# Kernel tuning notes

Measured on AMD Instinct MI355X. Metric: run time of the kernel, lower is better.

## Reference

```python
import jax, jax.numpy as jnp
import numpy as np

U, I, D = 100000, 50000, 64
N = U + I
E = 3_000_000
B = 8192
NEG_SLOPE = 0.2
REG_LAMBDA = 1e-4


def setup_inputs() -> dict:
    key = jax.random.key(0)
    ks = jax.random.split(key, 16)
    s = 0.05  # xavier-ish scale for params
    inp = {
        "user": jax.random.randint(ks[0], (B,), 0, U, dtype=jnp.int32),
        "positive": jax.random.randint(ks[1], (B,), 0, I, dtype=jnp.int32),
        "negative": jax.random.randint(ks[2], (B,), 0, I, dtype=jnp.int32),
        "rows": jax.random.randint(ks[3], (E,), 0, N, dtype=jnp.int32),
        "cols": jax.random.randint(ks[4], (E,), 0, N, dtype=jnp.int32),
        # normalized adjacency values are small positive numbers ~ 1/sqrt(du*di)
        "vals": jax.random.uniform(ks[5], (E,), dtype=jnp.float32) * 0.05,
        "user_emb": jax.random.normal(ks[6], (U, D), dtype=jnp.float32) * s,
        "item_emb": jax.random.normal(ks[7], (I, D), dtype=jnp.float32) * s,
        "W_gcn0": jax.random.normal(ks[8], (D, D), dtype=jnp.float32) * s,
        "b_gcn0": jax.random.normal(ks[9], (1, D), dtype=jnp.float32) * s,
        "W_mlp0": jax.random.normal(ks[10], (D, D), dtype=jnp.float32) * s,
        "b_mlp0": jax.random.normal(ks[11], (1, D), dtype=jnp.float32) * s,
        "W_gcn1": jax.random.normal(ks[12], (D, D), dtype=jnp.float32) * s,
        "b_gcn1": jax.random.normal(ks[13], (1, D), dtype=jnp.float32) * s,
        "W_mlp1": jax.random.normal(ks[14], (D, D), dtype=jnp.float32) * s,
        "b_mlp1": jax.random.normal(ks[15], (1, D), dtype=jnp.float32) * s,
    }
    return inp


def reference(user, positive, negative, rows, cols, vals,
              user_emb, item_emb,
              W_gcn0, b_gcn0, W_mlp0, b_mlp0,
              W_gcn1, b_gcn1, W_mlp1, b_mlp1):
    def spmm(x):  # sparse (N,N) @ dense (N,D) via COO gather + segment-sum
        return jax.ops.segment_sum(vals[:, None] * x[cols], rows, num_segments=N)

    ego = jnp.concatenate([user_emb, item_emb], axis=0)  # [N, D]
    all_embs = [ego]
    for W_g, b_g, W_m, b_m in ((W_gcn0, b_gcn0, W_mlp0, b_mlp0),
                               (W_gcn1, b_gcn1, W_mlp1, b_mlp1)):
        side = spmm(ego)
        gcn = jax.nn.leaky_relu(side @ W_g + b_g, negative_slope=NEG_SLOPE)
        ego = gcn @ W_m + b_m  # mess_dropout prob = 0 -> identity
        norm = jnp.linalg.norm(ego, axis=1, keepdims=True)
        all_embs.append(ego / jnp.maximum(norm, 1e-12))  # F.normalize p=2
    final = jnp.concatenate(all_embs, axis=1)  # [N, 3*D]
    users_e, items_e = final[:U], final[U:]

    u = users_e[user]
    p = items_e[positive]
    n = items_e[negative]
    pos_s = jnp.sum(u * p, axis=-1)
    neg_s = jnp.sum(u * n, axis=-1)
    bpr_loss = jnp.mean(jax.nn.softplus(neg_s - pos_s))  # -mean(logsigmoid(pos-neg))

    eu = user_emb[user]
    ep = item_emb[positive]
    en = item_emb[negative]
    reg = 0.5 * (jnp.sum(eu ** 2) + jnp.sum(ep ** 2) + jnp.sum(en ** 2)) / B
    reg_loss = REG_LAMBDA * reg
    return jnp.stack([bpr_loss, reg_loss])
```

## Files before the change

### kernel.cpp

```cpp
#include <hip/hip_runtime.h>
#include <math.h>

#define U_CNT 100000
#define I_CNT 50000
#define D_DIM 64
#define N_CNT 150000
#define B_CNT 8192
#define NEG_SLOPE 0.2f
#define REG_LAMBDA 1e-4f

#define RPB 128
#define NBK ((N_CNT + RPB - 1) / RPB)
#define CAP 4096

__device__ __forceinline__ float bf2f(unsigned short u) {
    return __uint_as_float((unsigned int)u << 16);
}
__device__ __forceinline__ unsigned short f2bf(float f) {
    unsigned int x = __float_as_uint(f);
    x += 0x7FFFu + ((x >> 16) & 1u);
    return (unsigned short)(x >> 16);
}

__global__ __launch_bounds__(256) void k_cvt(const float* __restrict__ uemb,
                                             const float* __restrict__ iemb,
                                             unsigned short* __restrict__ dst) {
    long long i = (long long)blockIdx.x * 256 + threadIdx.x;
    long long base = i * 8;
    const long long TOT = (long long)N_CNT * 64;
    if (base >= TOT) return;
    const long long USZ = (long long)U_CNT * 64;
    const float* s = (base < USZ) ? uemb + base : iemb + (base - USZ);
    float4 a = *(const float4*)s;
    float4 b = *(const float4*)(s + 4);
    union { unsigned short us[8]; uint4 v; } o;
    o.us[0] = f2bf(a.x); o.us[1] = f2bf(a.y); o.us[2] = f2bf(a.z); o.us[3] = f2bf(a.w);
    o.us[4] = f2bf(b.x); o.us[5] = f2bf(b.y); o.us[6] = f2bf(b.z); o.us[7] = f2bf(b.w);
    *(uint4*)(dst + base) = o.v;
}


__global__ __launch_bounds__(256) void k_bhist(const int* __restrict__ rows,
                                               int* __restrict__ bcnt, int E) {
    __shared__ int h[NBK];
    for (int i = threadIdx.x; i < NBK; i += 256) h[i] = 0;
    __syncthreads();
    int per = (E + gridDim.x - 1) / gridDim.x;
    int s = blockIdx.x * per, e = min(E, s + per);
    for (int i = s + threadIdx.x; i < e; i += 256) atomicAdd(&h[rows[i] >> 7], 1);
    __syncthreads();
    for (int i = threadIdx.x; i < NBK; i += 256) {
        int v = h[i];
        if (v) atomicAdd(&bcnt[i], v);
    }
}

__global__ void k_bscan(const int* __restrict__ bcnt, int* __restrict__ bb, int n) {
    __shared__ int lds[256];
    __shared__ int base;
    int tid = threadIdx.x;
    if (tid == 0) { base = 0; bb[0] = 0; }
    __syncthreads();
    for (int start = 0; start < n; start += 256) {
        int i = start + tid;
        int x = (i < n) ? bcnt[i] : 0;
        lds[tid] = x;
        __syncthreads();
        for (int off = 1; off < 256; off <<= 1) {
            int t = (tid >= off) ? lds[tid - off] : 0;
            __syncthreads();
            lds[tid] += t;
            __syncthreads();
        }
        if (i < n) bb[i + 1] = base + lds[tid];
        __syncthreads();
        if (tid == 0) base += lds[255];
        __syncthreads();
    }
}

__global__ __launch_bounds__(256) void k_bscatterA(const int* __restrict__ rows,
                                                   const int* __restrict__ cols,
                                                   const float* __restrict__ vals,
                                                   const int* __restrict__ bb,
                                                   int* __restrict__ bfill,
                                                   int2* __restrict__ edges, int E) {
    __shared__ int h[NBK];
    __shared__ int f[NBK];
    for (int i = threadIdx.x; i < NBK; i += 256) { h[i] = 0; f[i] = 0; }
    __syncthreads();
    int per = (E + gridDim.x - 1) / gridDim.x;
    int s = blockIdx.x * per, e = min(E, s + per);
    for (int i = s + threadIdx.x; i < e; i += 256) atomicAdd(&h[rows[i] >> 7], 1);
    __syncthreads();
    for (int i = threadIdx.x; i < NBK; i += 256) {
        int c = h[i];
        h[i] = c ? atomicAdd(&bfill[i], c) : 0;
    }
    __syncthreads();
    for (int i = s + threadIdx.x; i < e; i += 256) {
        int r = rows[i];
        int b = r >> 7, rl = r & 127;
        int pos = atomicAdd(&f[b], 1);
        int slot = bb[b] + h[b] + pos;
        edges[slot] = make_int2((rl << 18) | cols[i], __float_as_int(vals[i]));
    }
}

__global__ __launch_bounds__(256) void k_bfinal(int2* __restrict__ edges,
                                                const int* __restrict__ bb,
                                                int* __restrict__ rs, int E) {
    __shared__ int2 led[CAP];
    __shared__ int lcnt[RPB], lscan[RPB], lfill[RPB];
    int b = blockIdx.x;
    int s = bb[b], e = bb[b + 1];
    int nb = e - s;
    int tid = threadIdx.x;
    if (tid < RPB) { lcnt[tid] = 0; lfill[tid] = 0; }
    __syncthreads();
    for (int i = tid; i < nb; i += 256) {
        int2 ed = edges[s + i];
        if (i < CAP) led[i] = ed;
        atomicAdd(&lcnt[ed.x >> 18], 1);
    }
    __syncthreads();
    if (tid == 0) {
        int run = 0;
        for (int j = 0; j < RPB; ++j) { lscan[j] = run; run += lcnt[j]; }
    }
    __syncthreads();
    if (tid < RPB) {
        int row = b * RPB + tid;
        if (row < N_CNT) rs[row] = s + lscan[tid];
    }
    if (b == gridDim.x - 1 && tid == 0) rs[N_CNT] = E;
    int lim = min(nb, CAP);
    for (int i = tid; i < lim; i += 256) {
        int2 ed = led[i];
        int rl = ed.x >> 18;
        int pos = atomicAdd(&lfill[rl], 1);
        edges[s + lscan[rl] + pos] = make_int2(ed.x & 0x3FFFF, ed.y);
    }
    for (int base = CAP; base < nb; base += 256) {
        int i = base + tid;
        int2 ed;
        bool ok = (i < nb);
        if (ok) ed = edges[s + i];
        __syncthreads();
        if (ok) {
            int rl = ed.x >> 18;
            int pos = atomicAdd(&lfill[rl], 1);
            edges[s + lscan[rl] + pos] = make_int2(ed.x & 0x3FFFF, ed.y);
        }
        __syncthreads();
    }
}

__global__ void k_spmm(const int* __restrict__ rs, const int2* __restrict__ edges,
                       const unsigned short* __restrict__ src,
                       unsigned short* __restrict__ out_bf) {
    int gid = blockIdx.x * blockDim.x + threadIdx.x;
    int w = gid >> 6;
    int lane = gid & 63;
    if (w >= N_CNT) return;
    int s = rs[w], e = rs[w + 1];
    float acc = 0.f;
    int i = s;
    for (; i + 4 <= e; i += 4) {
        int2 e0 = edges[i], e1 = edges[i + 1], e2 = edges[i + 2], e3 = edges[i + 3];
        float a0 = bf2f(src[e0.x * 64 + lane]);
        float a1 = bf2f(src[e1.x * 64 + lane]);
        float a2 = bf2f(src[e2.x * 64 + lane]);
        float a3 = bf2f(src[e3.x * 64 + lane]);
        acc = fmaf(__int_as_float(e0.y), a0, acc);
        acc = fmaf(__int_as_float(e1.y), a1, acc);
        acc = fmaf(__int_as_float(e2.y), a2, acc);
        acc = fmaf(__int_as_float(e3.y), a3, acc);
    }
    for (; i < e; ++i) {
        int2 ed = edges[i];
        acc = fmaf(__int_as_float(ed.y), bf2f(src[ed.x * 64 + lane]), acc);
    }
    out_bf[(size_t)w * 64 + lane] = f2bf(acc);
}

template <int WRITE_BF>
__global__ __launch_bounds__(256, 1) void k_dense(const unsigned short* __restrict__ x_in,
                                                  const float* __restrict__ Wg,
                                                  const float* __restrict__ bg,
                                                  const float* __restrict__ Wm,
                                                  const float* __restrict__ bm,
                                                  float* __restrict__ out,
                                                  unsigned short* __restrict__ out_bf,
                                                  float* __restrict__ rnorm) {
    __shared__ __align__(16) float sWgT[4096];
    __shared__ __align__(16) float sWm[4096];
    __shared__ float sbg[64], sbm[64];
    int tid = threadIdx.x;
    for (int i = tid; i < 4096; i += 256) {
        int k = i >> 6, j = i & 63;
        sWgT[j * 64 + k] = Wg[i];
        sWm[i] = Wm[i];
    }
    if (tid < 64) {
        sbg[tid] = bg[tid];
        sbm[tid] = bm[tid];
    }
    __syncthreads();
    int r = blockIdx.x * 256 + tid;
    if (r >= N_CNT) return;

    float xr[64];
    const uint4* xp = (const uint4*)(x_in + (size_t)r * 64);
#pragma unroll
    for (int t = 0; t < 8; ++t) {
        uint4 q = xp[t];
        unsigned int u;
        u = q.x; xr[t * 8 + 0] = __uint_as_float(u << 16); xr[t * 8 + 1] = __uint_as_float(u & 0xFFFF0000u);
        u = q.y; xr[t * 8 + 2] = __uint_as_float(u << 16); xr[t * 8 + 3] = __uint_as_float(u & 0xFFFF0000u);
        u = q.z; xr[t * 8 + 4] = __uint_as_float(u << 16); xr[t * 8 + 5] = __uint_as_float(u & 0xFFFF0000u);
        u = q.w; xr[t * 8 + 6] = __uint_as_float(u << 16); xr[t * 8 + 7] = __uint_as_float(u & 0xFFFF0000u);
    }

    float z[64];
#pragma unroll
    for (int j = 0; j < 64; ++j) z[j] = sbm[j];

    for (int j = 0; j < 64; ++j) {
        float acc = sbg[j];
#pragma unroll
        for (int k = 0; k < 16; ++k) {
            float4 w = *(const float4*)&sWgT[j * 64 + k * 4];
            acc = fmaf(xr[k * 4 + 0], w.x, acc);
            acc = fmaf(xr[k * 4 + 1], w.y, acc);
            acc = fmaf(xr[k * 4 + 2], w.z, acc);
            acc = fmaf(xr[k * 4 + 3], w.w, acc);
        }
        float y = (acc >= 0.f) ? acc : NEG_SLOPE * acc;
#pragma unroll
        for (int k = 0; k < 16; ++k) {
            float4 w = *(const float4*)&sWm[j * 64 + k * 4];
            z[k * 4 + 0] = fmaf(y, w.x, z[k * 4 + 0]);
            z[k * 4 + 1] = fmaf(y, w.y, z[k * 4 + 1]);
            z[k * 4 + 2] = fmaf(y, w.z, z[k * 4 + 2]);
            z[k * 4 + 3] = fmaf(y, w.w, z[k * 4 + 3]);
        }
    }
    float nrm2 = 0.f;
#pragma unroll
    for (int j = 0; j < 64; ++j) nrm2 = fmaf(z[j], z[j], nrm2);
    float nrm = sqrtf(nrm2);
    float rn = 1.f / fmaxf(nrm, 1e-12f);
    rnorm[r] = rn;
    float4* op = (float4*)(out + (size_t)r * 64);
#pragma unroll
    for (int i = 0; i < 16; ++i) {
        float4 t;
        t.x = z[i * 4 + 0];
        t.y = z[i * 4 + 1];
        t.z = z[i * 4 + 2];
        t.w = z[i * 4 + 3];
        op[i] = t;
    }
    if (WRITE_BF) {
        uint4* bp = (uint4*)(out_bf + (size_t)r * 64);
#pragma unroll
        for (int t = 0; t < 8; ++t) {
            union { unsigned short us[8]; uint4 v; } o;
#pragma unroll
            for (int q = 0; q < 8; ++q) o.us[q] = f2bf(z[t * 8 + q]);
            bp[t] = o.v;
        }
    }
}

#define SCORE_BLOCKS 128
__global__ __launch_bounds__(256) void k_score(const int* __restrict__ user,
                                               const int* __restrict__ posi,
                                               const int* __restrict__ negi,
                                               const float* __restrict__ uemb,
                                               const float* __restrict__ iemb,
                                               const float* __restrict__ ego1,
                                               const float* __restrict__ rn1,
                                               const float* __restrict__ ego2,
                                               const float* __restrict__ rn2,
                                               float* __restrict__ out) {
    __shared__ float ssp[4], srg[4];
    int tid = threadIdx.x;
    int lane = tid & 63;
    int wv = tid >> 6;
    int gw = blockIdx.x * 4 + wv;
    const int NW = SCORE_BLOCKS * 4;

    float sp_acc = 0.f, rg_acc = 0.f;
    for (int w = gw; w < B_CNT; w += NW) {
        int iu = user[w], ip = posi[w], ineg = negi[w];
        size_t ru = (size_t)iu;
        size_t rp = (size_t)U_CNT + ip;
        size_t rn_ = (size_t)U_CNT + ineg;

        float u0 = uemb[(size_t)iu * 64 + lane];
        float p0 = iemb[(size_t)ip * 64 + lane];
        float n0 = iemb[(size_t)ineg * 64 + lane];
        float pos = u0 * p0;
        float neg = u0 * n0;
        float reg = u0 * u0 + p0 * p0 + n0 * n0;

        float a1 = rn1[ru], b1 = rn1[rp], c1 = rn1[rn_];
        float u1 = ego1[ru * 64 + lane] * a1;
        float p1 = ego1[rp * 64 + lane] * b1;
        float n1 = ego1[rn_ * 64 + lane] * c1;
        pos = fmaf(u1, p1, pos);
        neg = fmaf(u1, n1, neg);

        float a2 = rn2[ru], b2 = rn2[rp], c2 = rn2[rn_];
        float u2 = ego2[ru * 64 + lane] * a2;
        float p2 = ego2[rp * 64 + lane] * b2;
        float n2 = ego2[rn_ * 64 + lane] * c2;
        pos = fmaf(u2, p2, pos);
        neg = fmaf(u2, n2, neg);

#pragma unroll
        for (int off = 32; off; off >>= 1) {
            pos += __shfl_xor(pos, off);
            neg += __shfl_xor(neg, off);
            reg += __shfl_xor(reg, off);
        }
        float t = neg - pos;
        float sp = fmaxf(t, 0.f) + log1pf(expf(-fabsf(t)));
        sp_acc += sp;
        rg_acc += reg;
    }
    if (lane == 0) {
        ssp[wv] = sp_acc;
        srg[wv] = rg_acc;
    }
    __syncthreads();
    if (tid == 0) {
        float s = ssp[0] + ssp[1] + ssp[2] + ssp[3];
        float r = srg[0] + srg[1] + srg[2] + srg[3];
        atomicAdd(&out[0], s * (1.0f / B_CNT));
        atomicAdd(&out[1], r * (0.5f * REG_LAMBDA / B_CNT));
    }
}


static inline size_t alignup(size_t x) { return (x + 255) & ~(size_t)255; }

extern "C" void kernel_launch(void* const* d_in, const int* in_sizes, int n_in,
                              void* d_out, int out_size, void* d_ws, size_t ws_size,
                              hipStream_t stream) {
    const int* user = (const int*)d_in[0];
    const int* posi = (const int*)d_in[1];
    const int* negi = (const int*)d_in[2];
    const int* rows = (const int*)d_in[3];
    const int* cols = (const int*)d_in[4];
    const float* vals = (const float*)d_in[5];
    const float* uemb = (const float*)d_in[6];
    const float* iemb = (const float*)d_in[7];
    const float* Wg0 = (const float*)d_in[8];
    const float* bg0 = (const float*)d_in[9];
    const float* Wm0 = (const float*)d_in[10];
    const float* bm0 = (const float*)d_in[11];
    const float* Wg1 = (const float*)d_in[12];
    const float* bg1 = (const float*)d_in[13];
    const float* Wm1 = (const float*)d_in[14];
    const float* bm1 = (const float*)d_in[15];
    const int E = in_sizes[3];
    float* out = (float*)d_out;

    char* p = (char*)d_ws;
    auto take = [&](size_t bytes) -> char* {
        char* q = p;
        p += alignup(bytes);
        return q;
    };
    int* rs = (int*)take((size_t)(N_CNT + 1) * 4);
    int* bcnt = (int*)take((size_t)NBK * 4 * 2);
    int* bfill = bcnt + NBK;
    int* bb = (int*)take((size_t)(NBK + 1) * 4);
    int2* edges = (int2*)take((size_t)E * 8);
    unsigned short* ego0_bf = (unsigned short*)take((size_t)N_CNT * 64 * 2);
    unsigned short* side_bf = (unsigned short*)take((size_t)N_CNT * 64 * 2);
    unsigned short* ego1_bf = (unsigned short*)take((size_t)N_CNT * 64 * 2);
    float* ego1 = (float*)take((size_t)N_CNT * 64 * 4);
    float* ego2 = (float*)take((size_t)N_CNT * 64 * 4);
    float* rn1 = (float*)take((size_t)N_CNT * 4);
    float* rn2 = (float*)take((size_t)N_CNT * 4);

    hipMemsetAsync(out, 0, 2 * sizeof(float), stream);
    hipMemsetAsync(bcnt, 0, (size_t)NBK * 4 * 2, stream);

    const long long TOT = (long long)N_CNT * 64;
    int cb = (int)((TOT / 8 + 255) / 256);
    k_cvt<<<cb, 256, 0, stream>>>(uemb, iemb, ego0_bf);

    k_bhist<<<256, 256, 0, stream>>>(rows, bcnt, E);
    k_bscan<<<1, 256, 0, stream>>>(bcnt, bb, NBK);
    k_bscatterA<<<256, 256, 0, stream>>>(rows, cols, vals, bb, bfill, edges, E);
    k_bfinal<<<NBK, 256, 0, stream>>>(edges, bb, rs, E);

    int sb = (N_CNT * 64 + 255) / 256;
    int db = (N_CNT + 255) / 256;

    k_spmm<<<sb, 256, 0, stream>>>(rs, edges, ego0_bf, side_bf);
    k_dense<1><<<db, 256, 0, stream>>>(side_bf, Wg0, bg0, Wm0, bm0, ego1, ego1_bf, rn1);
    k_spmm<<<sb, 256, 0, stream>>>(rs, edges, ego1_bf, side_bf);
    k_dense<0><<<db, 256, 0, stream>>>(side_bf, Wg1, bg1, Wm1, bm1, ego2, (unsigned short*)nullptr, rn2);

    k_score<<<SCORE_BLOCKS, 256, 0, stream>>>(user, posi, negi, uemb, iemb,
                                              ego1, rn1, ego2, rn2, out);
}
```

Before: 637.9 us.

## Split SpMM wavefront into four edge groups with vectorized bf16 gathers

```diff
diff --git a/kernel.cpp b/kernel.cpp
--- a/kernel.cpp
+++ b/kernel.cpp
@@ -156,36 +156,50 @@
     }
 }
 
-__global__ void k_spmm(const int* __restrict__ rs, const int2* __restrict__ edges,
-                       const unsigned short* __restrict__ src,
-                       unsigned short* __restrict__ out_bf) {
+__global__ __launch_bounds__(256) void k_spmm(const int* __restrict__ rs,
+                                              const int2* __restrict__ edges,
+                                              const unsigned short* __restrict__ src,
+                                              unsigned short* __restrict__ out_bf) {
     int gid = blockIdx.x * blockDim.x + threadIdx.x;
     int w = gid >> 6;
-    int lane = gid & 63;
     if (w >= N_CNT) return;
+    int lane = threadIdx.x & 63;
+    int sub = lane >> 4;
+    int sl = lane & 15;
     int s = rs[w], e = rs[w + 1];
-    float acc = 0.f;
-    int i = s;
-    for (; i + 4 <= e; i += 4) {
-        int2 e0 = edges[i], e1 = edges[i + 1], e2 = edges[i + 2], e3 = edges[i + 3];
-        float a0 = bf2f(src[e0.x * 64 + lane]);
-        float a1 = bf2f(src[e1.x * 64 + lane]);
-        float a2 = bf2f(src[e2.x * 64 + lane]);
-        float a3 = bf2f(src[e3.x * 64 + lane]);
-        acc = fmaf(__int_as_float(e0.y), a0, acc);
-        acc = fmaf(__int_as_float(e1.y), a1, acc);
-        acc = fmaf(__int_as_float(e2.y), a2, acc);
-        acc = fmaf(__int_as_float(e3.y), a3, acc);
-    }
-    for (; i < e; ++i) {
-        int2 ed = edges[i];
-        acc = fmaf(__int_as_float(ed.y), bf2f(src[ed.x * 64 + lane]), acc);
-    }
-    out_bf[(size_t)w * 64 + lane] = f2bf(acc);
+
+    float a0 = 0.f, a1 = 0.f, a2 = 0.f, a3 = 0.f;
+
+    int idx = s + sub;
+    int2 cur = (idx < e) ? edges[idx] : make_int2(0, 0);
+    if (idx >= e) cur.y = 0;
+    for (int base = s; base < e; base += 4) {
+        int nidx = base + 4 + sub;
+        int2 nxt = make_int2(0, 0);
+        if (nidx < e) nxt = edges[nidx];
+        unsigned int col = (unsigned int)cur.x;
+        uint2 g = *(const uint2*)(src + (size_t)col * 64 + sl * 4);
+        float v = __int_as_float(cur.y);
+        a0 = fmaf(v, __uint_as_float(g.x << 16), a0);
+        a1 = fmaf(v, __uint_as_float(g.x & 0xFFFF0000u), a1);
+        a2 = fmaf(v, __uint_as_float(g.y << 16), a2);
+        a3 = fmaf(v, __uint_as_float(g.y & 0xFFFF0000u), a3);
+        cur = nxt;
+    }
+    a0 += __shfl_xor(a0, 16); a0 += __shfl_xor(a0, 32);
+    a1 += __shfl_xor(a1, 16); a1 += __shfl_xor(a1, 32);
+    a2 += __shfl_xor(a2, 16); a2 += __shfl_xor(a2, 32);
+    a3 += __shfl_xor(a3, 16); a3 += __shfl_xor(a3, 32);
+    if (sub == 0) {
+        union { unsigned short us[4]; uint2 u; } o;
+        o.us[0] = f2bf(a0); o.us[1] = f2bf(a1);
+        o.us[2] = f2bf(a2); o.us[3] = f2bf(a3);
+        *(uint2*)&out_bf[(size_t)w * 64 + sl * 4] = o.u;
+    }
 }
 
 template <int WRITE_BF>
-__global__ __launch_bounds__(256, 1) void k_dense(const unsigned short* __restrict__ x_in,
+__global__ __launch_bounds__(256, 2) void k_dense(const unsigned short* __restrict__ x_in,
                                                   const float* __restrict__ Wg,
                                                   const float* __restrict__ bg,
                                                   const float* __restrict__ Wm,
@@ -227,15 +241,16 @@
     for (int j = 0; j < 64; ++j) z[j] = sbm[j];
 
     for (int j = 0; j < 64; ++j) {
-        float acc = sbg[j];
+        float p0 = 0.f, p1 = 0.f, p2 = 0.f, p3 = 0.f;
 #pragma unroll
         for (int k = 0; k < 16; ++k) {
             float4 w = *(const float4*)&sWgT[j * 64 + k * 4];
-            acc = fmaf(xr[k * 4 + 0], w.x, acc);
-            acc = fmaf(xr[k * 4 + 1], w.y, acc);
-            acc = fmaf(xr[k * 4 + 2], w.z, acc);
-            acc = fmaf(xr[k * 4 + 3], w.w, acc);
-        }
+            p0 = fmaf(xr[k * 4 + 0], w.x, p0);
+            p1 = fmaf(xr[k * 4 + 1], w.y, p1);
+            p2 = fmaf(xr[k * 4 + 2], w.z, p2);
+            p3 = fmaf(xr[k * 4 + 3], w.w, p3);
+        }
+        float acc = sbg[j] + ((p0 + p1) + (p2 + p3));
         float y = (acc >= 0.f) ? acc : NEG_SLOPE * acc;
 #pragma unroll
         for (int k = 0; k < 16; ++k) {
```

Result: faster. 615.4 us (-3.5%).
